# Kernel tuning notes

Measured on AMD Instinct MI355X. Metric: run time of the kernel, lower is better.

## Reference

```python
import jax, jax.numpy as jnp
import numpy as np


def setup_inputs() -> dict:
    key = jax.random.key(0)
    kz, kh, k0 = jax.random.split(key, 3)
    B, C, D, H, W = 2, 96, 32, 32, 32
    z = jax.random.uniform(kz, (B, C, D, H, W), dtype=jnp.float32)  # gate in [0,1]
    h_tilde = jax.random.normal(kh, (B, C, D, H, W), dtype=jnp.float32)  # candidate state
    h0 = jax.random.uniform(k0, (1,), dtype=jnp.float32)  # scalar initial state
    return {"z": z, "h_tilde": h_tilde, "h0": h0}


def reference(z, h_tilde, h0):
    """GruDirection3d with d1=d2=d3=1 (forward_3, no flips).

    The three wavefront slice-updates in the torch code jointly implement
        out[d, y, x] = z[d, y, x] * h_tilde[d, y, x]
                       + (1 - z[d, y, x]) * out[d-1, y-1, x-1]
    with out == h0 whenever any index goes below 0 (the padded border).
    We realize it as t_num = min(D, H, W) full-volume shifted updates: after
    iteration k, all voxels with min(d, y, x) <= k-1 hold their final value,
    so after t_num iterations the result matches the torch wavefront DP exactly.
    """
    B, C, D, H, W = z.shape
    t_num = min(D, H, W)  # static shapes -> python int, jit-safe
    # padded state: index 0 along each spatial axis is the h0 border (never written)
    h_pad = jnp.full((B, C, D + 1, H + 1, W + 1), h0[0], dtype=z.dtype)

    one = jnp.asarray(1, dtype=z.dtype)

    def step(h_pad, _):
        prev = h_pad[:, :, :-1, :-1, :-1]  # out[d-1, y-1, x-1] (with border = h0)
        new = z * h_tilde + (one - z) * prev
        return h_pad.at[:, :, 1:, 1:, 1:].set(new), None

    h_pad, _ = jax.lax.scan(step, h_pad, None, length=t_num)
    return h_pad[:, :, 1:, 1:, 1:]
```

## Files before the change

### kernel.cpp

```cpp
#include <hip/hip_runtime.h>
#include <hip/hip_bf16.h>


#define PLANE 1024
#define DD 32

__global__ __launch_bounds__(1024) void gru3d_wavefront(
    const float* __restrict__ z,
    const float* __restrict__ ht,
    const float* __restrict__ h0p,
    float* __restrict__ out)
{
    __shared__ float buf[2][PLANE];

    const int bc  = blockIdx.x;
    const int tid = threadIdx.x;
    const int y   = tid >> 5;
    const int x   = tid & 31;
    const float h0 = h0p[0];

    const float* zb = z   + (size_t)bc * (DD * PLANE);
    const float* tb = ht  + (size_t)bc * (DD * PLANE);
    float*       ob = out + (size_t)bc * (DD * PLANE);

    float zA = zb[tid];
    float tA = tb[tid];
    float zB = zb[PLANE + tid];
    float tB = tb[PLANE + tid];

    float h = zA * tA + (1.0f - zA) * h0;
    ob[tid] = h;
    buf[0][tid] = h;
    __syncthreads();

    const bool interior = (y > 0) & (x > 0);

    #pragma unroll 4
    for (int d = 1; d < DD; ++d) {
        zA = zB; tA = tB;
        if (d + 1 < DD) {
            zB = zb[(d + 1) * PLANE + tid];
            tB = tb[(d + 1) * PLANE + tid];
        }
        float pv = interior ? buf[(d - 1) & 1][tid - 33] : h0;
        float hn = zA * tA + (1.0f - zA) * pv;
        ob[d * PLANE + tid] = hn;
        buf[d & 1][tid] = hn;
        __syncthreads();
    }
}

extern "C" void kernel_launch(void* const* d_in, const int* in_sizes, int n_in,
                              void* d_out, int out_size, void* d_ws, size_t ws_size,
                              hipStream_t stream) {
    const float* z  = (const float*)d_in[0];
    const float* ht = (const float*)d_in[1];
    const float* h0 = (const float*)d_in[2];
    float* out      = (float*)d_out;

    const int BC = 2 * 96;
    gru3d_wavefront<<<dim3(BC), dim3(1024), 0, stream>>>(z, ht, h0, out);
}
```

Before: 99.77 us.

## Use float2 per-thread work, 512 threads, deeper prefetch and lighter barriers

Each thread now handles two adjacent x positions loaded as float2. The block shrinks to 512 threads and the loads run two planes ahead instead of one. Shared memory rows are padded to 33 floats, and __syncthreads is replaced by an inline s_waitcnt lgkmcnt(0) plus s_barrier. The goal is more memory-level parallelism and less barrier and instruction overhead per plane along the serial depth loop. The cost is more registers per thread and reliance on the hand-written barrier for LDS ordering.

```diff
diff --git a/kernel.cpp b/kernel.cpp
--- a/kernel.cpp
+++ b/kernel.cpp
@@ -2,51 +2,68 @@
 #include <hip/hip_bf16.h>
 
 
-#define PLANE 1024
-#define DD 32
+#define P2   512
+#define DD   32
+#define ROWP 33
 
-__global__ __launch_bounds__(1024) void gru3d_wavefront(
+#define BAR() asm volatile("s_waitcnt lgkmcnt(0)\n\ts_barrier" ::: "memory")
+
+__global__ __launch_bounds__(512) void gru3d_wf2(
     const float* __restrict__ z,
     const float* __restrict__ ht,
     const float* __restrict__ h0p,
     float* __restrict__ out)
 {
-    __shared__ float buf[2][PLANE];
+    __shared__ float buf[2][32 * ROWP];
 
     const int bc  = blockIdx.x;
     const int tid = threadIdx.x;
-    const int y   = tid >> 5;
-    const int x   = tid & 31;
+    const int y   = tid >> 4;
+    const int xt  = tid & 15;
+    const int x0  = xt * 2;
     const float h0 = h0p[0];
 
-    const float* zb = z   + (size_t)bc * (DD * PLANE);
-    const float* tb = ht  + (size_t)bc * (DD * PLANE);
-    float*       ob = out + (size_t)bc * (DD * PLANE);
+    const size_t slab = (size_t)bc * (DD * 2 * P2);
+    const float2* zv = (const float2*)(z  + slab);
+    const float2* tv = (const float2*)(ht + slab);
+    float2*       ov = (float2*)(out + slab);
+    const int off = y * 16 + xt;
 
-    float zA = zb[tid];
-    float tA = tb[tid];
-    float zB = zb[PLANE + tid];
-    float tB = tb[PLANE + tid];
+    float2 zA = zv[off],          tA = tv[off];
+    float2 zB = zv[P2 + off],     tB = tv[P2 + off];
+    float2 zC = zv[2 * P2 + off], tC = tv[2 * P2 + off];
 
-    float h = zA * tA + (1.0f - zA) * h0;
-    ob[tid] = h;
-    buf[0][tid] = h;
-    __syncthreads();
+    float2 h;
+    h.x = zA.x * tA.x + (1.0f - zA.x) * h0;
+    h.y = zA.y * tA.y + (1.0f - zA.y) * h0;
+    ov[off] = h;
+    buf[0][y * ROWP + x0]     = h.x;
+    buf[0][y * ROWP + x0 + 1] = h.y;
+    BAR();
 
-    const bool interior = (y > 0) & (x > 0);
+    for (int d = 1; d < DD; ++d) {
+        const int dn = (d + 2 < DD) ? (d + 2) : (DD - 1);
+        float2 zN = zv[dn * P2 + off], tN = tv[dn * P2 + off];
 
-    #pragma unroll 4
-    for (int d = 1; d < DD; ++d) {
-        zA = zB; tA = tB;
-        if (d + 1 < DD) {
-            zB = zb[(d + 1) * PLANE + tid];
-            tB = tb[(d + 1) * PLANE + tid];
+        const float* pb = buf[(d - 1) & 1];
+        float2 pv;
+        if (y > 0) {
+            pv.x = (x0 > 0) ? pb[(y - 1) * ROWP + x0 - 1] : h0;
+            pv.y = pb[(y - 1) * ROWP + x0];
+        } else {
+            pv.x = h0; pv.y = h0;
         }
-        float pv = interior ? buf[(d - 1) & 1][tid - 33] : h0;
-        float hn = zA * tA + (1.0f - zA) * pv;
-        ob[d * PLANE + tid] = hn;
-        buf[d & 1][tid] = hn;
-        __syncthreads();
+
+        h.x = zB.x * tB.x + (1.0f - zB.x) * pv.x;
+        h.y = zB.y * tB.y + (1.0f - zB.y) * pv.y;
+        ov[d * P2 + off] = h;
+
+        float* cb = buf[d & 1];
+        cb[y * ROWP + x0]     = h.x;
+        cb[y * ROWP + x0 + 1] = h.y;
+
+        zB = zC; tB = tC; zC = zN; tC = tN;
+        BAR();
     }
 }
 
@@ -59,5 +76,5 @@
     float* out      = (float*)d_out;
 
     const int BC = 2 * 96;
-    gru3d_wavefront<<<dim3(BC), dim3(1024), 0, stream>>>(z, ht, h0, out);
+    gru3d_wf2<<<dim3(BC), dim3(512), 0, stream>>>(z, ht, h0, out);
 }
```

New measurement: 104.7 us. +5.0%, slower.

## Replace shared-memory wavefront with single-wave register kernel using lane shuffles

Applied to the files above, without the earlier changes.

Each block now runs one 64-lane wave where every lane holds 16 contiguous voxels of a plane in registers. The diagonal predecessor is fetched via __shfl_up instead of shared memory, removing all block barriers. z and h_tilde are prefetched two slices ahead with float4 loads. This trades far fewer threads per CU, and therefore less latency hiding, for no synchronization overhead.

```diff
diff --git a/kernel.cpp b/kernel.cpp
--- a/kernel.cpp
+++ b/kernel.cpp
@@ -2,51 +2,90 @@
 #include <hip/hip_bf16.h>
 
 
-#define PLANE 1024
 #define DD 32
 
-__global__ __launch_bounds__(1024) void gru3d_wavefront(
-    const float* __restrict__ z,
-    const float* __restrict__ ht,
+#define UNPACK16(dst, src)                                                   \
+    dst[0]=src[0].x;  dst[1]=src[0].y;  dst[2]=src[0].z;  dst[3]=src[0].w;   \
+    dst[4]=src[1].x;  dst[5]=src[1].y;  dst[6]=src[1].z;  dst[7]=src[1].w;   \
+    dst[8]=src[2].x;  dst[9]=src[2].y;  dst[10]=src[2].z; dst[11]=src[2].w;  \
+    dst[12]=src[3].x; dst[13]=src[3].y; dst[14]=src[3].z; dst[15]=src[3].w;
+
+__global__ __launch_bounds__(64) void gru3d_reg(
+    const float* __restrict__ zg,
+    const float* __restrict__ tg,
     const float* __restrict__ h0p,
-    float* __restrict__ out)
+    float* __restrict__ og)
 {
-    __shared__ float buf[2][PLANE];
-
-    const int bc  = blockIdx.x;
-    const int tid = threadIdx.x;
-    const int y   = tid >> 5;
-    const int x   = tid & 31;
+    const int L  = threadIdx.x;
+    const int bc = blockIdx.x;
+    const int xh = L & 1;
+    const bool top = (L < 2);
     const float h0 = h0p[0];
 
-    const float* zb = z   + (size_t)bc * (DD * PLANE);
-    const float* tb = ht  + (size_t)bc * (DD * PLANE);
-    float*       ob = out + (size_t)bc * (DD * PLANE);
+    const size_t b4 = (size_t)bc * (DD * 256) + (size_t)L * 4;
+    const float4* zv = (const float4*)zg + b4;
+    const float4* tv = (const float4*)tg + b4;
+    float4*       ov = (float4*)og + b4;
 
-    float zA = zb[tid];
-    float tA = tb[tid];
-    float zB = zb[PLANE + tid];
-    float tB = tb[PLANE + tid];
+    float4 zq[3][4], tq[3][4];
+    #pragma unroll
+    for (int p = 0; p < 3; ++p) {
+        #pragma unroll
+        for (int i = 0; i < 4; ++i) {
+            zq[p][i] = zv[p * 256 + i];
+            tq[p][i] = tv[p * 256 + i];
+        }
+    }
 
-    float h = zA * tA + (1.0f - zA) * h0;
-    ob[tid] = h;
-    buf[0][tid] = h;
-    __syncthreads();
+    float h[16];
 
-    const bool interior = (y > 0) & (x > 0);
+    {
+        float zc[16], tc[16];
+        UNPACK16(zc, zq[0]); UNPACK16(tc, tq[0]);
+        #pragma unroll
+        for (int i = 0; i < 16; ++i)
+            h[i] = zc[i] * tc[i] + (1.0f - zc[i]) * h0;
+        #pragma unroll
+        for (int i = 0; i < 4; ++i)
+            ov[i] = make_float4(h[4*i], h[4*i+1], h[4*i+2], h[4*i+3]);
+    }
 
-    #pragma unroll 4
+    #pragma unroll
     for (int d = 1; d < DD; ++d) {
-        zA = zB; tA = tB;
-        if (d + 1 < DD) {
-            zB = zb[(d + 1) * PLANE + tid];
-            tB = tb[(d + 1) * PLANE + tid];
+        const int cur = d % 3;
+        const int nxt = (d + 2) % 3;
+        if (d + 2 < DD) {
+            #pragma unroll
+            for (int i = 0; i < 4; ++i) {
+                zq[nxt][i] = zv[(d + 2) * 256 + i];
+                tq[nxt][i] = tv[(d + 2) * 256 + i];
+            }
         }
-        float pv = interior ? buf[(d - 1) & 1][tid - 33] : h0;
-        float hn = zA * tA + (1.0f - zA) * pv;
-        ob[d * PLANE + tid] = hn;
-        buf[d & 1][tid] = hn;
-        __syncthreads();
+
+        float s[16];
+        #pragma unroll
+        for (int i = 0; i < 16; ++i) s[i] = __shfl_up(h[i], 2, 64);
+        float bnd = __shfl_up(h[15], 3, 64);
+
+        float zc[16], tc[16];
+        UNPACK16(zc, zq[cur]); UNPACK16(tc, tq[cur]);
+
+        float hn[16];
+        {
+            float pv0 = top ? h0 : (xh ? bnd : h0);
+            hn[0] = zc[0] * tc[0] + (1.0f - zc[0]) * pv0;
+        }
+        #pragma unroll
+        for (int i = 1; i < 16; ++i) {
+            float pv = top ? h0 : s[i - 1];
+            hn[i] = zc[i] * tc[i] + (1.0f - zc[i]) * pv;
+        }
+        #pragma unroll
+        for (int i = 0; i < 16; ++i) h[i] = hn[i];
+
+        #pragma unroll
+        for (int i = 0; i < 4; ++i)
+            ov[d * 256 + i] = make_float4(h[4*i], h[4*i+1], h[4*i+2], h[4*i+3]);
     }
 }
 
@@ -59,5 +98,5 @@
     float* out      = (float*)d_out;
 
     const int BC = 2 * 96;
-    gru3d_wavefront<<<dim3(BC), dim3(1024), 0, stream>>>(z, ht, h0, out);
+    gru3d_reg<<<dim3(BC), dim3(64), 0, stream>>>(z, ht, h0, out);
 }
```

Result: slower. 103.6 us (+3.8%).

## Stream z/h_tilde planes into LDS via async DMA ring with 256-thread blocks

Applied to the files above, without the earlier changes.

Replaces the 1024-thread per-plane kernel with 256 threads that each handle four x-values per plane. Input planes are prefetched five deep into a six-slot LDS ring using global_load_lds DMA, with manual vmcnt waits. The previous hidden-state plane lives in a padded (pitch 33) LDS buffer whose border is preset to h0, which removes the interior branch. Outputs are written as float4. The goal is to hide global load latency across the serial depth recurrence and cut per-thread overhead. The cost is more LDS use and fragile hand-counted waitcnt values.

```diff
diff --git a/kernel.cpp b/kernel.cpp
--- a/kernel.cpp
+++ b/kernel.cpp
@@ -2,52 +2,86 @@
 #include <hip/hip_bf16.h>
 
 
-#define PLANE 1024
-#define DD 32
+#define NPLANE 32
+#define PITCH  33
 
-__global__ __launch_bounds__(1024) void gru3d_wavefront(
-    const float* __restrict__ z,
-    const float* __restrict__ ht,
+__device__ __forceinline__ void dma16(const float* gp, float* lp) {
+    __builtin_amdgcn_global_load_lds(
+        (const __attribute__((address_space(1))) void*)gp,
+        (__attribute__((address_space(3))) void*)lp, 16, 0, 0);
+}
+
+#define WAITV(N) asm volatile("s_waitcnt vmcnt(" #N ")" ::: "memory")
+#define BARL()   asm volatile("s_waitcnt lgkmcnt(0)\n\ts_barrier" ::: "memory")
+
+__global__ __launch_bounds__(256) void gru3d_dma4(
+    const float* __restrict__ zg,
+    const float* __restrict__ tg,
     const float* __restrict__ h0p,
-    float* __restrict__ out)
+    float* __restrict__ og)
 {
-    __shared__ float buf[2][PLANE];
+    __shared__ float rz[6][1024];
+    __shared__ float rt[6][1024];
+    __shared__ float hb[2][PITCH * 33];
 
+    const int tid = threadIdx.x;
+    const int w   = tid >> 6;
+    const int l   = tid & 63;
     const int bc  = blockIdx.x;
-    const int tid = threadIdx.x;
-    const int y   = tid >> 5;
-    const int x   = tid & 31;
+    const int u   = l >> 3;
+    const int r   = 8 * w + u;
+    const int x0  = (l & 7) * 4;
     const float h0 = h0p[0];
 
-    const float* zb = z   + (size_t)bc * (DD * PLANE);
-    const float* tb = ht  + (size_t)bc * (DD * PLANE);
-    float*       ob = out + (size_t)bc * (DD * PLANE);
+    const size_t slab = (size_t)bc * (NPLANE * 1024);
+    const float* zb = zg + slab;
+    const float* tb = tg + slab;
+    float4*      ov = (float4*)(og + slab);
 
-    float zA = zb[tid];
-    float tA = tb[tid];
-    float zB = zb[PLANE + tid];
-    float tB = tb[PLANE + tid];
+    #define ISSUE(p) do {                                            \
+        const int _s = (p) % 6;                                      \
+        dma16(zb + (p) * 1024 + w * 256 + l * 4, &rz[_s][w * 256]);  \
+        dma16(tb + (p) * 1024 + w * 256 + l * 4, &rt[_s][w * 256]);  \
+    } while (0)
 
-    float h = zA * tA + (1.0f - zA) * h0;
-    ob[tid] = h;
-    buf[0][tid] = h;
-    __syncthreads();
+    ISSUE(0); ISSUE(1); ISSUE(2); ISSUE(3); ISSUE(4);
 
-    const bool interior = (y > 0) & (x > 0);
+    for (int i = tid; i < 2 * PITCH * 33; i += 256)
+        ((float*)hb)[i] = h0;
+    BARL();
 
-    #pragma unroll 4
-    for (int d = 1; d < DD; ++d) {
-        zA = zB; tA = tB;
-        if (d + 1 < DD) {
-            zB = zb[(d + 1) * PLANE + tid];
-            tB = tb[(d + 1) * PLANE + tid];
-        }
-        float pv = interior ? buf[(d - 1) & 1][tid - 33] : h0;
-        float hn = zA * tA + (1.0f - zA) * pv;
-        ob[d * PLANE + tid] = hn;
-        buf[d & 1][tid] = hn;
-        __syncthreads();
-    }
+    #define CONSUME(d) do {                                              \
+        const float4 zq = ((const float4*)&rz[(d) % 6][0])[w * 64 + l];  \
+        const float4 tq = ((const float4*)&rt[(d) % 6][0])[w * 64 + l];  \
+        const float* pb = hb[((d) + 1) & 1];                             \
+        float*       cb = hb[(d) & 1];                                   \
+        float4 o;                                                        \
+        o.x = zq.x * tq.x + (1.0f - zq.x) * pb[r * PITCH + x0 + 0];      \
+        o.y = zq.y * tq.y + (1.0f - zq.y) * pb[r * PITCH + x0 + 1];      \
+        o.z = zq.z * tq.z + (1.0f - zq.z) * pb[r * PITCH + x0 + 2];      \
+        o.w = zq.w * tq.w + (1.0f - zq.w) * pb[r * PITCH + x0 + 3];      \
+        cb[(r + 1) * PITCH + x0 + 1] = o.x;                              \
+        cb[(r + 1) * PITCH + x0 + 2] = o.y;                              \
+        cb[(r + 1) * PITCH + x0 + 3] = o.z;                              \
+        cb[(r + 1) * PITCH + x0 + 4] = o.w;                              \
+        ov[(d) * 256 + w * 64 + l] = o;                                  \
+        BARL();                                                          \
+    } while (0)
+
+    #define RND(d, N) do { if ((d) + 5 < NPLANE) ISSUE((d) + 5);  \
+                           WAITV(N); CONSUME(d); } while (0)
+
+    RND(0, 10); RND(1, 11); RND(2, 12); RND(3, 13); RND(4, 14);
+    RND(5, 15); RND(6, 15); RND(7, 15); RND(8, 15); RND(9, 15);
+    RND(10, 15); RND(11, 15); RND(12, 15); RND(13, 15); RND(14, 15);
+    RND(15, 15); RND(16, 15); RND(17, 15); RND(18, 15); RND(19, 15);
+    RND(20, 15); RND(21, 15); RND(22, 15); RND(23, 15); RND(24, 15);
+    RND(25, 15); RND(26, 15);
+    RND(27, 13); RND(28, 11); RND(29, 9); RND(30, 7); RND(31, 5);
+
+    #undef RND
+    #undef CONSUME
+    #undef ISSUE
 }
 
 extern "C" void kernel_launch(void* const* d_in, const int* in_sizes, int n_in,
@@ -59,5 +93,5 @@
     float* out      = (float*)d_out;
 
     const int BC = 2 * 96;
-    gru3d_wavefront<<<dim3(BC), dim3(1024), 0, stream>>>(z, ht, h0, out);
+    gru3d_dma4<<<dim3(BC), dim3(256), 0, stream>>>(z, ht, h0, out);
 }
```

Measured after the change: 104.3 us. +4.5%, slower.
